# Performance work log

Hardware: AMD Instinct MI355X
Metric: run time of the kernel (lower is better)

## Reference

```python
import jax, jax.numpy as jnp
import numpy as np

EMBED_DIM = 300
HIDDEN = 128
N_CLS = 20
N_NODES = 100000
N_EDGES = 1600000
N_GRAPHS = 512
EPSILON = 1e-06


def setup_inputs() -> dict:
    key = jax.random.key(0)
    ks = jax.random.split(key, 10)
    x_fp16 = jax.random.normal(ks[0], (N_NODES, EMBED_DIM), dtype=jnp.float16)
    ei = jax.random.randint(ks[1], (2, N_EDGES), 0, N_NODES, dtype=jnp.int32)
    batch = jnp.sort(jax.random.randint(ks[2], (N_NODES,), 0, N_GRAPHS, dtype=jnp.int32))
    mask = jax.random.randint(ks[3], (N_NODES,), 0, 2, dtype=jnp.int32).astype(jnp.bool_)
    def glorot(k, fan_in, fan_out):
        s = (6.0 / (fan_in + fan_out)) ** 0.5
        return jax.random.uniform(k, (fan_in, fan_out), jnp.float32, -s, s)
    return {
        "x_fp16": x_fp16, "ei": ei, "batch": batch, "mask": mask,
        "W1": glorot(ks[4], EMBED_DIM, HIDDEN), "b1": jnp.zeros((HIDDEN,), jnp.float32),
        "W2": glorot(ks[5], HIDDEN, HIDDEN), "b2": jnp.zeros((HIDDEN,), jnp.float32),
        "Wout": glorot(ks[6], HIDDEN, N_CLS), "bout": jnp.zeros((N_CLS,), jnp.float32),
    }


def gcn_conv(x, W, b, src, dst, n):
    # PyG GCNConv: x' = D^{-1/2} (A + I) D^{-1/2} (x W) + b
    h = x @ W  # [N, out]
    loop = jnp.arange(n, dtype=src.dtype)
    s = jnp.concatenate([src, loop])
    d = jnp.concatenate([dst, loop])
    deg = jax.ops.segment_sum(jnp.ones_like(d, dtype=h.dtype), d, num_segments=n)
    dinv = jax.lax.rsqrt(deg)  # deg >= 1 thanks to self-loops
    norm = dinv[s] * dinv[d]  # [E+N]
    msg = h[s] * norm[:, None]
    return jax.ops.segment_sum(msg, d, num_segments=n) + b


def reference(x_fp16, ei, batch, mask, W1, b1, W2, b2, Wout, bout):
    n = x_fp16.shape[0]
    src, dst = ei[0], ei[1]
    x = x_fp16.astype(jnp.float32)
    x = jax.nn.relu(gcn_conv(x, W1, b1, src, dst, n))
    x = jax.nn.relu(gcn_conv(x, W2, b2, src, dst, n))
    m = mask.astype(jnp.float32)[:, None]  # [N,1]
    ent_sum = jax.ops.segment_sum(x * m, batch, num_segments=N_GRAPHS)  # [G,H]
    ent_cnt = jax.ops.segment_sum(m, batch, num_segments=N_GRAPHS)  # [G,1]
    doc_vec = ent_sum / (ent_cnt + EPSILON)
    # fallback: mean over all nodes when a graph has no masked entities
    node_sum = jax.ops.segment_sum(x, batch, num_segments=N_GRAPHS)
    node_cnt = jax.ops.segment_sum(jnp.ones((n, 1), jnp.float32), batch, num_segments=N_GRAPHS)
    mean_pool = node_sum / jnp.maximum(node_cnt, 1.0)
    zero = ent_cnt < EPSILON  # [G,1]
    doc_vec = jnp.where(zero, mean_pool, doc_vec)
    return jax.nn.log_softmax(doc_vec @ Wout + bout, axis=1)
```

## Files before the change

kernel.cpp:

```cpp
#include <hip/hip_runtime.h>
#include <hip/hip_fp16.h>

#define NN 100000
#define NE 1600000
#define DIM 300
#define HID 128
#define NC 20
#define NG 512
#define NBK 196
#define BCH 4096

typedef _Float16 h8 __attribute__((ext_vector_type(8)));
typedef float f4 __attribute__((ext_vector_type(4)));

union pack16 { float4 v; __half2 h2[4]; };

__device__ __forceinline__ __half tohalf(float v) {
  if (!(v == v)) v = 0.f;
  v = fminf(fmaxf(v, -60000.f), 60000.f);
  return __float2half(v);
}

__device__ __forceinline__ float load_x(const void* xraw, size_t o, int mode) {
  float v;
  if (mode == 2) v = ((const float*)xraw)[o];
  else {
    unsigned short u = ((const unsigned short*)xraw)[o];
    if (mode == 1) { union { unsigned w; float f; } c; c.w = ((unsigned)u) << 16; v = c.f; }
    else { union { unsigned short s; _Float16 h; } c; c.s = u; v = (float)c.h; }
  }
  if (!(v == v)) v = 0.f;
  return fminf(fmaxf(v, -1e4f), 1e4f);
}


__global__ void k_probe_modes(const unsigned short* __restrict__ xu, unsigned* __restrict__ diag) {
  int b = blockIdx.x, t = threadIdx.x;
  int mode = b % 3, chunk = b / 3;
  float m = 0.f;
  if (mode == 0) {
    int base = chunk * 16384;
    for (int j = t; j < 16384; j += 256) {
      union { unsigned short s; _Float16 h; } c; c.s = xu[base + j];
      float v = fabsf((float)c.h);
      if (v == v && v < 65000.f) m = fmaxf(m, v);
    }
  } else if (mode == 1) {
    int base = chunk * 16384;
    for (int j = t; j < 16384; j += 256) {
      union { unsigned w; float f; } c; c.w = ((unsigned)xu[base + j]) << 16;
      float v = fabsf(c.f);
      if (v == v && v < 1e30f) m = fmaxf(m, v);
    }
  } else {
    const float* xf = (const float*)xu;
    int base = chunk * 8192;
    for (int j = t; j < 8192; j += 256) {
      float v = fabsf(xf[base + j]);
      if (v == v && v < 1e30f) m = fmaxf(m, v);
    }
  }
  for (int off = 32; off; off >>= 1) m = fmaxf(m, __shfl_xor(m, off));
  if ((t & 63) == 0) atomicMax(&diag[20 + mode], __float_as_uint(m));
}

__global__ void k_probe_umax(const unsigned* __restrict__ p, unsigned* __restrict__ slot) {
  __shared__ unsigned red[256];
  int t = threadIdx.x; unsigned m = 0;
  for (int j = t; j < 25000; j += 256) m = max(m, p[j]);
  red[t] = m; __syncthreads();
  for (int off = 128; off; off >>= 1) { if (t < off) red[t] = max(red[t], red[t + off]); __syncthreads(); }
  if (t == 0) *slot = red[0];
}

__global__ void k_probe_ei(const int* __restrict__ e32, unsigned* __restrict__ slot) {
  int i = blockIdx.x * blockDim.x + threadIdx.x;
  int stride = gridDim.x * blockDim.x;
  unsigned z = 0;
  for (; i < 50000; i += stride) if (e32[2 * i + 1] == 0) z++;
  atomicAdd(slot, z);
}

__global__ void k_decide(const unsigned* __restrict__ diag, int* __restrict__ flags) {
  float M16 = __uint_as_float(diag[20]);
  float M32 = __uint_as_float(diag[21]);
  float Mf  = __uint_as_float(diag[22]);
  int xmode = 3;
  if      (Mf  > 3.f && Mf  < 8.f) xmode = 2;
  else if (M32 > 3.f && M32 < 8.f) xmode = 1;
  else if (M16 > 3.f && M16 < 8.f) xmode = 0;
  flags[0] = xmode;
  unsigned uA = diag[24], uB = diag[25];
  bool Ab = (uA >= 32u && uA < 1024u), Bb = (uB >= 32u && uB < 1024u);
  int swap = -1;
  if (Ab && !Bb) swap = 0;
  else if (Bb && !Ab) swap = 1;
  int mint = -1;
  if (swap >= 0) {
    unsigned um = (swap == 0) ? uB : uA;
    if (um <= 1u) mint = 1;
    else if (um >= 65536u) mint = 0;
  }
  flags[2] = (swap == 1) ? 1 : 0;
  flags[1] = (mint == 1) ? 1 : 0;
  flags[4] = (swap >= 0 && mint >= 0) ? 1 : 0;
  flags[3] = (diag[26] >= 49990u) ? 1 : 0;
}


__global__ void k_bhist(const int* __restrict__ e32, const int* __restrict__ flags,
                        int* __restrict__ bcnt) {
  __shared__ int hist[NBK];
  int e64 = flags[3];
  int t = threadIdx.x;
  for (int j = t; j < NBK; j += 256) hist[j] = 0;
  __syncthreads();
  int i = blockIdx.x * blockDim.x + t;
  int stride = gridDim.x * blockDim.x;
  for (; i < NE; i += stride) {
    int s = e64 ? e32[2 * i] : e32[i];
    int d = e64 ? e32[2 * NE + 2 * i] : e32[NE + i];
    if ((unsigned)s < (unsigned)NN && (unsigned)d < (unsigned)NN)
      atomicAdd(&hist[d >> 9], 1);
  }
  __syncthreads();
  for (int j = t; j < NBK; j += 256) if (hist[j]) atomicAdd(&bcnt[j], hist[j]);
}

__global__ void k_bscan(const int* __restrict__ bcnt, int* __restrict__ boff,
                        int* __restrict__ bcur) {
  if (blockIdx.x == 0 && threadIdx.x == 0) {
    int run = 0;
    for (int j = 0; j < NBK; j++) { boff[j] = run; bcur[j] = run; run += bcnt[j]; }
    boff[NBK] = run;
  }
}

__global__ __launch_bounds__(256)
void k_bscatter(const int* __restrict__ e32, const int* __restrict__ flags,
                int* __restrict__ bcur, unsigned* __restrict__ ebuf) {
  __shared__ uint2 stage[BCH];
  __shared__ int hist[NBK];
  __shared__ int lbase[NBK];
  __shared__ int lcur[NBK];
  int e64 = flags[3];
  int t = threadIdx.x;
  for (int j = t; j < NBK; j += 256) { hist[j] = 0; lcur[j] = 0; }
  __syncthreads();
  int start = blockIdx.x * BCH;
  int n = NE - start; if (n > BCH) n = BCH;
  for (int i = t; i < n; i += 256) {
    int idx = start + i;
    int s = e64 ? e32[2 * idx] : e32[idx];
    int d = e64 ? e32[2 * NE + 2 * idx] : e32[NE + idx];
    bool ok = ((unsigned)s < (unsigned)NN) && ((unsigned)d < (unsigned)NN);
    stage[i] = make_uint2(ok ? (unsigned)s : 0xFFFFFFFFu, (unsigned)(ok ? d : 0));
    if (ok) atomicAdd(&hist[d >> 9], 1);
  }
  __syncthreads();
  for (int j = t; j < NBK; j += 256) if (hist[j] > 0) lbase[j] = atomicAdd(&bcur[j], hist[j]);
  __syncthreads();
  for (int i = t; i < n; i += 256) {
    unsigned s = stage[i].x;
    if (s == 0xFFFFFFFFu) continue;
    int d = (int)stage[i].y;
    int b = d >> 9;
    int o = atomicAdd(&lcur[b], 1);
    ebuf[lbase[b] + o] = (s << 9) | (unsigned)(d & 511);
  }
}

__global__ __launch_bounds__(256)
void k_bfinal(const unsigned* __restrict__ ebuf, const int* __restrict__ boff,
              int* __restrict__ row_off, float* __restrict__ dinv, int* __restrict__ csr) {
  __shared__ int ldeg[512];
  __shared__ int lcur[512];
  int b = blockIdx.x, t = threadIdx.x;
  int base = b * 512;
  int nn = NN - base; if (nn > 512) nn = 512;
  for (int j = t; j < 512; j += 256) ldeg[j] = 0;
  __syncthreads();
  int s0 = boff[b], s1 = boff[b + 1];
  for (int e = s0 + t; e < s1; e += 256) atomicAdd(&ldeg[ebuf[e] & 511], 1);
  __syncthreads();
  if (t == 0) {
    int run = s0;
    for (int i = 0; i < nn; i++) { lcur[i] = run; row_off[base + i] = run; run += ldeg[i]; }
    if (b == gridDim.x - 1) row_off[NN] = run;
  }
  __syncthreads();
  for (int j = t; j < nn; j += 256) dinv[base + j] = rsqrtf((float)ldeg[j] + 1.0f);
  for (int e = s0 + t; e < s1; e += 256) {
    unsigned v = ebuf[e];
    int p = atomicAdd(&lcur[v & 511], 1);
    csr[p] = (int)(v >> 9);
  }
}


__global__ void k_gstart(const int* __restrict__ A, const int* __restrict__ B,
                         const int* __restrict__ flags, int* __restrict__ gstart) {
  const int* batch = flags[2] ? B : A;
  int g = blockIdx.x * blockDim.x + threadIdx.x;
  if (g > NG) return;
  if (g == NG) { gstart[NG] = NN; return; }
  int lo = 0, hi = NN;
  while (lo < hi) { int mid = (lo + hi) >> 1; if (batch[mid] < g) lo = mid + 1; else hi = mid; }
  gstart[g] = lo;
}


__global__ void k_prep(const float* __restrict__ W1, const float* __restrict__ W2,
                       _Float16* __restrict__ w1f, _Float16* __restrict__ w2f) {
  int idx = blockIdx.x * blockDim.x + threadIdx.x;
  const int S1 = 10 * 8 * 64 * 8;
  const int S2 = 4 * 8 * 64 * 8;
  if (idx < S1) {
    int j = idx & 7, l = (idx >> 3) & 63, nt = (idx >> 9) & 7, kc = idx >> 12;
    int k = kc * 32 + ((l >> 4) << 3) + j;
    int n = nt * 16 + (l & 15);
    w1f[idx] = (k < DIM) ? (_Float16)W1[k * HID + n] : (_Float16)0.f;
  } else if (idx < S1 + S2) {
    int q = idx - S1;
    int j = q & 7, l = (q >> 3) & 63, nt = (q >> 9) & 7, kc = q >> 12;
    int k = kc * 32 + ((l >> 4) << 3) + j;
    int n = nt * 16 + (l & 15);
    w2f[q] = (_Float16)W2[k * HID + n];
  }
}


#define XST 328

__global__ __launch_bounds__(256)
void k_gemm1_mfma(const void* __restrict__ Ain, const _Float16* __restrict__ bfrag,
                  const float* __restrict__ dinv, const int* __restrict__ flags,
                  __half* __restrict__ outg) {
  __shared__ _Float16 xs[64 * XST];
  const int mode = flags[0] & 3;
  int tid = threadIdx.x;
  int w = tid >> 6, l = tid & 63;
  int rowbase = blockIdx.x * 64;
  int k0base = (l >> 4) << 3;
  int cb = l & 15;

  for (int t = tid; t < 640; t += 256) {
    int rl = t / 10, j = t - rl * 10;
    *(unsigned*)&xs[rl * XST + 300 + j * 2] = 0u;
  }

  if (mode == 2) {
    const float* xf = (const float*)Ain;
    for (int c = tid; c < 64 * 75; c += 256) {
      int rl = c / 75, k = (c - rl * 75) * 4;
      int r = rowbase + rl;
      _Float16 o0 = 0, o1 = 0, o2 = 0, o3 = 0;
      if (r < NN) {
        float4 fv = *(const float4*)(xf + (size_t)r * DIM + k);
        o0 = (_Float16)fv.x; o1 = (_Float16)fv.y; o2 = (_Float16)fv.z; o3 = (_Float16)fv.w;
      }
      _Float16* p = &xs[rl * XST + k];
      p[0] = o0; p[1] = o1; p[2] = o2; p[3] = o3;
    }
  } else {
    const unsigned short* xu = (const unsigned short*)Ain;
    uint2 regs[19];
    #pragma unroll
    for (int it = 0; it < 19; it++) {
      int c = tid + it * 256;
      uint2 u = make_uint2(0u, 0u);
      if (c < 64 * 75) {
        int rl = c / 75, k = (c - rl * 75) * 4;
        int r = rowbase + rl;
        if (r < NN) u = *(const uint2*)(xu + (size_t)r * DIM + k);
      }
      regs[it] = u;
    }
    __builtin_amdgcn_sched_barrier(0);
    #pragma unroll
    for (int it = 0; it < 19; it++) {
      int c = tid + it * 256;
      if (c >= 64 * 75) continue;
      int rl = c / 75, k = (c - rl * 75) * 4;
      uint2 u = regs[it];
      unsigned short s0 = u.x & 0xFFFF, s1 = u.x >> 16, s2 = u.y & 0xFFFF, s3 = u.y >> 16;
      _Float16 o0, o1, o2, o3;
      if (mode == 1) {
        union { unsigned w_; float f; } c0, c1, c2, c3;
        c0.w_ = ((unsigned)s0) << 16; c1.w_ = ((unsigned)s1) << 16;
        c2.w_ = ((unsigned)s2) << 16; c3.w_ = ((unsigned)s3) << 16;
        o0 = (_Float16)c0.f; o1 = (_Float16)c1.f; o2 = (_Float16)c2.f; o3 = (_Float16)c3.f;
      } else {
        union { unsigned short s; _Float16 h; } d0, d1, d2, d3;
        d0.s = s0; d1.s = s1; d2.s = s2; d3.s = s3;
        o0 = d0.h; o1 = d1.h; o2 = d2.h; o3 = d3.h;
      }
      _Float16* p = &xs[rl * XST + k];
      p[0] = o0; p[1] = o1; p[2] = o2; p[3] = o3;
    }
  }
  __syncthreads();

  f4 acc[4][2];
  f4 zero = {0.f, 0.f, 0.f, 0.f};
  #pragma unroll
  for (int rg = 0; rg < 4; rg++) { acc[rg][0] = zero; acc[rg][1] = zero; }

  #pragma unroll
  for (int kc = 0; kc < 10; kc++) {
    int ko = kc * 32 + k0base;
    h8 a0 = *(const h8*)&xs[(0 * 16 + cb) * XST + ko];
    h8 a1 = *(const h8*)&xs[(1 * 16 + cb) * XST + ko];
    h8 a2 = *(const h8*)&xs[(2 * 16 + cb) * XST + ko];
    h8 a3 = *(const h8*)&xs[(3 * 16 + cb) * XST + ko];
    #pragma unroll
    for (int ntl = 0; ntl < 2; ntl++) {
      int nt = w * 2 + ntl;
      h8 bv = *(const h8*)&bfrag[(((kc << 3) + nt) * 64 + l) * 8];
      acc[0][ntl] = __builtin_amdgcn_mfma_f32_16x16x32_f16(a0, bv, acc[0][ntl], 0, 0, 0);
      acc[1][ntl] = __builtin_amdgcn_mfma_f32_16x16x32_f16(a1, bv, acc[1][ntl], 0, 0, 0);
      acc[2][ntl] = __builtin_amdgcn_mfma_f32_16x16x32_f16(a2, bv, acc[2][ntl], 0, 0, 0);
      acc[3][ntl] = __builtin_amdgcn_mfma_f32_16x16x32_f16(a3, bv, acc[3][ntl], 0, 0, 0);
    }
  }

  int rquad = (l >> 4) << 2;
  #pragma unroll
  for (int rg = 0; rg < 4; rg++) {
    #pragma unroll
    for (int i = 0; i < 4; i++) {
      int r = rowbase + rg * 16 + rquad + i;
      if (r >= NN) continue;
      float dv = dinv[r];
      __half* orow = outg + (size_t)r * HID;
      orow[(w * 2 + 0) * 16 + cb] = tohalf(acc[rg][0][i] * dv);
      orow[(w * 2 + 1) * 16 + cb] = tohalf(acc[rg][1][i] * dv);
    }
  }
}


__global__ __launch_bounds__(256)
void k_gemm2_mfma(const __half* __restrict__ Ain, const _Float16* __restrict__ bfrag,
                  const float* __restrict__ dinv, __half* __restrict__ outg) {
  __shared__ _Float16 xs[64 * 136];
  int tid = threadIdx.x;
  int w = tid >> 6, l = tid & 63;
  int rowbase = blockIdx.x * 64;
  int k0base = (l >> 4) << 3;
  int cb = l & 15;

  {
    h8 regs[4];
    #pragma unroll
    for (int it = 0; it < 4; it++) {
      int c = tid + it * 256;
      int rl = c >> 4, k = (c & 15) * 8;
      int r = rowbase + rl;
      h8 v = {};
      if (r < NN) v = *(const h8*)((const _Float16*)Ain + (size_t)r * HID + k);
      regs[it] = v;
    }
    __builtin_amdgcn_sched_barrier(0);
    #pragma unroll
    for (int it = 0; it < 4; it++) {
      int c = tid + it * 256;
      int rl = c >> 4, k = (c & 15) * 8;
      *(h8*)&xs[rl * 136 + k] = regs[it];
    }
  }
  __syncthreads();

  f4 acc[4][2];
  f4 zero = {0.f, 0.f, 0.f, 0.f};
  #pragma unroll
  for (int rg = 0; rg < 4; rg++) { acc[rg][0] = zero; acc[rg][1] = zero; }

  #pragma unroll
  for (int kc = 0; kc < 4; kc++) {
    int ko = kc * 32 + k0base;
    h8 a0 = *(const h8*)&xs[(0 * 16 + cb) * 136 + ko];
    h8 a1 = *(const h8*)&xs[(1 * 16 + cb) * 136 + ko];
    h8 a2 = *(const h8*)&xs[(2 * 16 + cb) * 136 + ko];
    h8 a3 = *(const h8*)&xs[(3 * 16 + cb) * 136 + ko];
    #pragma unroll
    for (int ntl = 0; ntl < 2; ntl++) {
      int nt = w * 2 + ntl;
      h8 bv = *(const h8*)&bfrag[(((kc << 3) + nt) * 64 + l) * 8];
      acc[0][ntl] = __builtin_amdgcn_mfma_f32_16x16x32_f16(a0, bv, acc[0][ntl], 0, 0, 0);
      acc[1][ntl] = __builtin_amdgcn_mfma_f32_16x16x32_f16(a1, bv, acc[1][ntl], 0, 0, 0);
      acc[2][ntl] = __builtin_amdgcn_mfma_f32_16x16x32_f16(a2, bv, acc[2][ntl], 0, 0, 0);
      acc[3][ntl] = __builtin_amdgcn_mfma_f32_16x16x32_f16(a3, bv, acc[3][ntl], 0, 0, 0);
    }
  }

  int rquad = (l >> 4) << 2;
  #pragma unroll
  for (int rg = 0; rg < 4; rg++) {
    #pragma unroll
    for (int i = 0; i < 4; i++) {
      int r = rowbase + rg * 16 + rquad + i;
      if (r >= NN) continue;
      float dv = dinv[r];
      __half* orow = outg + (size_t)r * HID;
      orow[(w * 2 + 0) * 16 + cb] = tohalf(acc[rg][0][i] * dv);
      orow[(w * 2 + 1) * 16 + cb] = tohalf(acc[rg][1][i] * dv);
    }
  }
}


__global__ __launch_bounds__(256)
void k_agg(const __half* __restrict__ g, const float* __restrict__ dinv,
           const int* __restrict__ row_off, const int* __restrict__ csr,
           const float* __restrict__ bias, __half* __restrict__ out) {
  int tid = threadIdx.x;
  int node = blockIdx.x * 4 + (tid >> 6);
  int l = tid & 63;
  if (node >= NN) return;
  int grp = l >> 4;
  int cl  = l & 15;
  size_t coff = (size_t)cl * 8;

  float a0 = 0.f, a1 = 0.f, a2 = 0.f, a3 = 0.f, a4 = 0.f, a5 = 0.f, a6 = 0.f, a7 = 0.f;
  pack16 r;

  #define ACCUM() do { \
    float2 f0 = __half22float2(r.h2[0]); \
    float2 f1 = __half22float2(r.h2[1]); \
    float2 f2 = __half22float2(r.h2[2]); \
    float2 f3 = __half22float2(r.h2[3]); \
    a0 += f0.x; a1 += f0.y; a2 += f1.x; a3 += f1.y; \
    a4 += f2.x; a5 += f2.y; a6 += f3.x; a7 += f3.y; } while (0)

  int e0 = row_off[node], e1 = row_off[node + 1];
  int e = e0 + grp;
  for (; e + 4 < e1; e += 8) {
    int s1 = csr[e], s2 = csr[e + 4];
    pack16 rA, rB;
    rA.v = *(const float4*)(g + (size_t)s1 * HID + coff);
    rB.v = *(const float4*)(g + (size_t)s2 * HID + coff);
    r = rA; ACCUM();
    r = rB; ACCUM();
  }
  if (e < e1) {
    int s1 = csr[e];
    r.v = *(const float4*)(g + (size_t)s1 * HID + coff);
    ACCUM();
  }
  if (grp == 0) {
    r.v = *(const float4*)(g + (size_t)node * HID + coff);
    ACCUM();
  }
  #undef ACCUM

  a0 += __shfl_xor(a0, 16); a1 += __shfl_xor(a1, 16); a2 += __shfl_xor(a2, 16); a3 += __shfl_xor(a3, 16);
  a4 += __shfl_xor(a4, 16); a5 += __shfl_xor(a5, 16); a6 += __shfl_xor(a6, 16); a7 += __shfl_xor(a7, 16);
  a0 += __shfl_xor(a0, 32); a1 += __shfl_xor(a1, 32); a2 += __shfl_xor(a2, 32); a3 += __shfl_xor(a3, 32);
  a4 += __shfl_xor(a4, 32); a5 += __shfl_xor(a5, 32); a6 += __shfl_xor(a6, 32); a7 += __shfl_xor(a7, 32);

  if (grp == 0) {
    float di = dinv[node];
    const float* bp = bias + coff;
    pack16 w;
    w.h2[0] = __floats2half2_rn(fmaxf(a0 * di + bp[0], 0.f), fmaxf(a1 * di + bp[1], 0.f));
    w.h2[1] = __floats2half2_rn(fmaxf(a2 * di + bp[2], 0.f), fmaxf(a3 * di + bp[3], 0.f));
    w.h2[2] = __floats2half2_rn(fmaxf(a4 * di + bp[4], 0.f), fmaxf(a5 * di + bp[5], 0.f));
    w.h2[3] = __floats2half2_rn(fmaxf(a6 * di + bp[6], 0.f), fmaxf(a7 * di + bp[7], 0.f));
    *(float4*)(out + (size_t)node * HID + coff) = w.v;
  }
}


__global__ __launch_bounds__(256)
void k_pool(const __half* __restrict__ o2, const void* __restrict__ Araw, const void* __restrict__ Braw,
            const int* __restrict__ gstart, const int* __restrict__ flags,
            float* __restrict__ doc) {
  __shared__ float lex[4][HID];
  __shared__ float lnx[4][HID];
  __shared__ int lec[4];
  int gid = blockIdx.x, tid = threadIdx.x;
  int wv = tid >> 6, l = tid & 63;
  int grp = l >> 4, cl = l & 15;
  size_t coff = (size_t)cl * 8;
  const int mint = flags[1];
  const void* mraw = flags[2] ? Araw : Braw;
  const unsigned char* m8 = (const unsigned char*)mraw;
  const int* m32 = (const int*)mraw;
  int s = gstart[gid], e = gstart[gid + 1];

  float ex[8], nx[8];
  #pragma unroll
  for (int j = 0; j < 8; j++) { ex[j] = 0.f; nx[j] = 0.f; }
  int ec = 0;

  for (int n = s + wv * 4 + grp; n < e; n += 16) {
    pack16 r;
    r.v = *(const float4*)(o2 + (size_t)n * HID + coff);
    float2 f0 = __half22float2(r.h2[0]);
    float2 f1 = __half22float2(r.h2[1]);
    float2 f2 = __half22float2(r.h2[2]);
    float2 f3 = __half22float2(r.h2[3]);
    float t0 = f0.x, t1 = f0.y, t2 = f1.x, t3 = f1.y;
    float t4 = f2.x, t5 = f2.y, t6 = f3.x, t7 = f3.y;
    nx[0] += t0; nx[1] += t1; nx[2] += t2; nx[3] += t3;
    nx[4] += t4; nx[5] += t5; nx[6] += t6; nx[7] += t7;
    bool mv = mint ? (m32[n] != 0) : (m8[n] != 0);
    if (mv) {
      ex[0] += t0; ex[1] += t1; ex[2] += t2; ex[3] += t3;
      ex[4] += t4; ex[5] += t5; ex[6] += t6; ex[7] += t7;
      ec++;
    }
  }
  #pragma unroll
  for (int j = 0; j < 8; j++) {
    ex[j] += __shfl_xor(ex[j], 16); ex[j] += __shfl_xor(ex[j], 32);
    nx[j] += __shfl_xor(nx[j], 16); nx[j] += __shfl_xor(nx[j], 32);
  }
  ec += __shfl_xor(ec, 16); ec += __shfl_xor(ec, 32);

  if (grp == 0) {
    #pragma unroll
    for (int j = 0; j < 8; j++) { lex[wv][cl * 8 + j] = ex[j]; lnx[wv][cl * 8 + j] = nx[j]; }
    if (cl == 0) lec[wv] = ec;
  }
  __syncthreads();
  if (tid < HID) {
    float exT = lex[0][tid] + lex[1][tid] + lex[2][tid] + lex[3][tid];
    float nxT = lnx[0][tid] + lnx[1][tid] + lnx[2][tid] + lnx[3][tid];
    int ecT = lec[0] + lec[1] + lec[2] + lec[3];
    int cnt = e - s;
    float dv;
    if (ecT > 0) dv = exT / ((float)ecT + 1e-6f);
    else dv = (cnt > 0) ? nxT / (float)cnt : 0.f;
    doc[gid * HID + tid] = dv;
  }
}

__global__ __launch_bounds__(64)
void k_out(const float* __restrict__ doc, const float* __restrict__ Wout,
           const float* __restrict__ bout, float* __restrict__ out) {
  __shared__ float dv[HID];
  int gid = blockIdx.x, l = threadIdx.x;
  dv[l] = doc[gid * HID + l];
  dv[l + 64] = doc[gid * HID + l + 64];
  __syncthreads();
  float logit = -1e30f;
  if (l < NC) {
    float acc = bout[l];
    for (int k = 0; k < HID; k++) acc += dv[k] * Wout[k * NC + l];
    logit = acc;
  }
  float m = logit;
  for (int off = 32; off; off >>= 1) m = fmaxf(m, __shfl_xor(m, off));
  float ex = (l < NC) ? expf(logit - m) : 0.f;
  float ssum = ex;
  for (int off = 32; off; off >>= 1) ssum += __shfl_xor(ssum, off);
  if (l < NC) out[gid * NC + l] = (logit - m) - logf(ssum);
}

__global__ void k_fail(float* __restrict__ out, float enc) {
  int i = blockIdx.x * blockDim.x + threadIdx.x;
  if (i < NG * NC) out[i] = -enc;
}


extern "C" void kernel_launch(void* const* d_in, const int* in_sizes, int n_in,
                              void* d_out, int out_size, void* d_ws, size_t ws_size,
                              hipStream_t stream) {
  int ix = -1, iei = -1, iA = -1, iB = -1, iW1 = -1, ib1 = -1, iW2 = -1, ib2 = -1, iWo = -1, ibo = -1;
  for (int i = 0; i < n_in; i++) {
    int s = in_sizes[i];
    if (s == 30000000) ix = i;
    else if (s == 3200000) iei = i;
    else if (s == 100000) { if (iA < 0) iA = i; else iB = i; }
    else if (s == 38400) iW1 = i;
    else if (s == 16384) iW2 = i;
    else if (s == 2560) iWo = i;
    else if (s == 20) ibo = i;
    else if (s == 128) { if (ib1 < 0) ib1 = i; else ib2 = i; }
  }
  float* out = (float*)d_out;
  int miss = -1;
  if (ix < 0) miss = 0; else if (iei < 0) miss = 1; else if (iA < 0 || iB < 0) miss = 2;
  else if (iW1 < 0) miss = 3; else if (ib1 < 0 || ib2 < 0) miss = 4; else if (iW2 < 0) miss = 5;
  else if (iWo < 0) miss = 6; else if (ibo < 0) miss = 7;
  if (miss >= 0) {
    k_fail<<<(NG * NC + 255) / 256, 256, 0, stream>>>(out, 8192.f + 64.f * (float)miss);
    return;
  }
  const void* x = d_in[ix];
  const int* e32 = (const int*)d_in[iei];
  const void* Araw = d_in[iA];
  const void* Braw = d_in[iB];
  const float* W1 = (const float*)d_in[iW1];
  const float* b1 = (const float*)d_in[ib1];
  const float* W2 = (const float*)d_in[iW2];
  const float* b2 = (const float*)d_in[ib2];
  const float* Wout = (const float*)d_in[iWo];
  const float* bout = (const float*)d_in[ibo];

  char* ws = (char*)d_ws;
  size_t off = 0;
  auto alloc = [&](size_t bytes) -> char* {
    char* p = ws + off; off += (bytes + 255) & ~(size_t)255; return p;
  };
  float* dinv   = (float*)alloc((size_t)NN * 4);
  int* row_off  = (int*)alloc((size_t)(NN + 1) * 4);
  int* csr      = (int*)alloc((size_t)NE * 4);
  int* bcnt     = (int*)alloc((size_t)NBK * 4);
  int* boff     = (int*)alloc((size_t)(NBK + 1) * 4);
  int* bcur     = (int*)alloc((size_t)NBK * 4);
  int* gstart   = (int*)alloc((size_t)(NG + 1) * 4);
  int* flags    = (int*)alloc(8 * 4);
  _Float16* w1f = (_Float16*)alloc(40960 * 2);
  _Float16* w2f = (_Float16*)alloc(16384 * 2);
  __half* gbuf  = (__half*)alloc((size_t)NN * HID * 2);
  __half* obuf  = (__half*)alloc((size_t)NN * HID * 2);
  float* doc    = (float*)alloc((size_t)NG * HID * 4);
  unsigned* diag = (unsigned*)alloc(64 * 4);
  unsigned* ebuf = (unsigned*)gbuf;

  hipMemsetAsync(bcnt, 0, (size_t)NBK * 4, stream);
  hipMemsetAsync(diag, 0, 64 * 4, stream);

  k_probe_modes<<<96, 256, 0, stream>>>((const unsigned short*)x, diag);
  k_probe_umax<<<1, 256, 0, stream>>>((const unsigned*)Araw, &diag[24]);
  k_probe_umax<<<1, 256, 0, stream>>>((const unsigned*)Braw, &diag[25]);
  k_probe_ei<<<64, 256, 0, stream>>>(e32, &diag[26]);
  k_decide<<<1, 1, 0, stream>>>(diag, flags);

  k_prep<<<(57344 + 255) / 256, 256, 0, stream>>>(W1, W2, w1f, w2f);
  k_bhist<<<1024, 256, 0, stream>>>(e32, flags, bcnt);
  k_bscan<<<1, 64, 0, stream>>>(bcnt, boff, bcur);
  k_bscatter<<<(NE + BCH - 1) / BCH, 256, 0, stream>>>(e32, flags, bcur, ebuf);
  k_bfinal<<<NBK, 256, 0, stream>>>(ebuf, boff, row_off, dinv, csr);
  k_gstart<<<(NG + 1 + 63) / 64, 64, 0, stream>>>((const int*)Araw, (const int*)Braw, flags, gstart);

  k_gemm1_mfma<<<(NN + 63) / 64, 256, 0, stream>>>(x, w1f, dinv, flags, gbuf);
  k_agg<<<NN / 4, 256, 0, stream>>>(gbuf, dinv, row_off, csr, b1, obuf);
  k_gemm2_mfma<<<(NN + 63) / 64, 256, 0, stream>>>(obuf, w2f, dinv, gbuf);
  k_agg<<<NN / 4, 256, 0, stream>>>(gbuf, dinv, row_off, csr, b2, obuf);

  k_pool<<<NG, 256, 0, stream>>>(obuf, Araw, Braw, gstart, flags, doc);
  k_out<<<NG, 64, 0, stream>>>(doc, Wout, bout, out);
}
```

Before: 355.2 us.

## Split gemm1 K dimension into two LDS halves to halve shared memory

The first-layer MFMA GEMM now stages the 300-wide input row tile in two halves (160 then 140 plus zero padding) through a half-size LDS buffer, with an extra barrier between phases. This cuts LDS per block roughly in half, and drops the 19-register prefetch array, so more blocks can be resident per CU to hide global load latency. In exchange, the second half's loads are serialized behind the first half's MFMAs, and the preload-all-then-convert scheme that batched global loads is gone.

```diff
diff --git a/kernel.cpp b/kernel.cpp
--- a/kernel.cpp
+++ b/kernel.cpp
@@ -31,6 +31,26 @@
   }
   if (!(v == v)) v = 0.f;
   return fminf(fmaxf(v, -1e4f), 1e4f);
+}
+
+__device__ __forceinline__ void cvt4(const void* Ain, size_t off, int mode, _Float16* o) {
+  if (mode == 2) {
+    float4 fv = *(const float4*)((const float*)Ain + off);
+    o[0] = (_Float16)fv.x; o[1] = (_Float16)fv.y; o[2] = (_Float16)fv.z; o[3] = (_Float16)fv.w;
+  } else {
+    uint2 u = *(const uint2*)((const unsigned short*)Ain + off);
+    unsigned short s0 = u.x & 0xFFFF, s1 = u.x >> 16, s2 = u.y & 0xFFFF, s3 = u.y >> 16;
+    if (mode == 1) {
+      union { unsigned w; float f; } c0, c1, c2, c3;
+      c0.w = ((unsigned)s0) << 16; c1.w = ((unsigned)s1) << 16;
+      c2.w = ((unsigned)s2) << 16; c3.w = ((unsigned)s3) << 16;
+      o[0] = (_Float16)c0.f; o[1] = (_Float16)c1.f; o[2] = (_Float16)c2.f; o[3] = (_Float16)c3.f;
+    } else {
+      union { unsigned short s; _Float16 h; } d0, d1, d2, d3;
+      d0.s = s0; d1.s = s1; d2.s = s2; d3.s = s3;
+      o[0] = d0.h; o[1] = d1.h; o[2] = d2.h; o[3] = d3.h;
+    }
+  }
 }
 
 
@@ -230,13 +250,13 @@
 }
 
 
-#define XST 328
+#define XS1 168
 
 __global__ __launch_bounds__(256)
 void k_gemm1_mfma(const void* __restrict__ Ain, const _Float16* __restrict__ bfrag,
                   const float* __restrict__ dinv, const int* __restrict__ flags,
                   __half* __restrict__ outg) {
-  __shared__ _Float16 xs[64 * XST];
+  __shared__ _Float16 xs[64 * XS1];
   const int mode = flags[0] & 3;
   int tid = threadIdx.x;
   int w = tid >> 6, l = tid & 63;
@@ -244,75 +264,65 @@
   int k0base = (l >> 4) << 3;
   int cb = l & 15;
 
-  for (int t = tid; t < 640; t += 256) {
-    int rl = t / 10, j = t - rl * 10;
-    *(unsigned*)&xs[rl * XST + 300 + j * 2] = 0u;
-  }
-
-  if (mode == 2) {
-    const float* xf = (const float*)Ain;
-    for (int c = tid; c < 64 * 75; c += 256) {
-      int rl = c / 75, k = (c - rl * 75) * 4;
-      int r = rowbase + rl;
-      _Float16 o0 = 0, o1 = 0, o2 = 0, o3 = 0;
-      if (r < NN) {
-        float4 fv = *(const float4*)(xf + (size_t)r * DIM + k);
-        o0 = (_Float16)fv.x; o1 = (_Float16)fv.y; o2 = (_Float16)fv.z; o3 = (_Float16)fv.w;
-      }
-      _Float16* p = &xs[rl * XST + k];
-      p[0] = o0; p[1] = o1; p[2] = o2; p[3] = o3;
-    }
-  } else {
-    const unsigned short* xu = (const unsigned short*)Ain;
-    uint2 regs[19];
-    #pragma unroll
-    for (int it = 0; it < 19; it++) {
-      int c = tid + it * 256;
-      uint2 u = make_uint2(0u, 0u);
-      if (c < 64 * 75) {
-        int rl = c / 75, k = (c - rl * 75) * 4;
-        int r = rowbase + rl;
-        if (r < NN) u = *(const uint2*)(xu + (size_t)r * DIM + k);
-      }
-      regs[it] = u;
-    }
-    __builtin_amdgcn_sched_barrier(0);
-    #pragma unroll
-    for (int it = 0; it < 19; it++) {
-      int c = tid + it * 256;
-      if (c >= 64 * 75) continue;
-      int rl = c / 75, k = (c - rl * 75) * 4;
-      uint2 u = regs[it];
-      unsigned short s0 = u.x & 0xFFFF, s1 = u.x >> 16, s2 = u.y & 0xFFFF, s3 = u.y >> 16;
-      _Float16 o0, o1, o2, o3;
-      if (mode == 1) {
-        union { unsigned w_; float f; } c0, c1, c2, c3;
-        c0.w_ = ((unsigned)s0) << 16; c1.w_ = ((unsigned)s1) << 16;
-        c2.w_ = ((unsigned)s2) << 16; c3.w_ = ((unsigned)s3) << 16;
-        o0 = (_Float16)c0.f; o1 = (_Float16)c1.f; o2 = (_Float16)c2.f; o3 = (_Float16)c3.f;
-      } else {
-        union { unsigned short s; _Float16 h; } d0, d1, d2, d3;
-        d0.s = s0; d1.s = s1; d2.s = s2; d3.s = s3;
-        o0 = d0.h; o1 = d1.h; o2 = d2.h; o3 = d3.h;
-      }
-      _Float16* p = &xs[rl * XST + k];
-      p[0] = o0; p[1] = o1; p[2] = o2; p[3] = o3;
-    }
-  }
-  __syncthreads();
-
   f4 acc[4][2];
   f4 zero = {0.f, 0.f, 0.f, 0.f};
   #pragma unroll
   for (int rg = 0; rg < 4; rg++) { acc[rg][0] = zero; acc[rg][1] = zero; }
 
   #pragma unroll
-  for (int kc = 0; kc < 10; kc++) {
+  for (int it = 0; it < 10; it++) {
+    int c = tid + it * 256;
+    int rl = c / 40, kk = (c - rl * 40) * 4;
+    int r = rowbase + rl;
+    _Float16 o[4] = {0, 0, 0, 0};
+    if (r < NN) cvt4(Ain, (size_t)r * DIM + kk, mode, o);
+    _Float16* p = &xs[rl * XS1 + kk];
+    p[0] = o[0]; p[1] = o[1]; p[2] = o[2]; p[3] = o[3];
+  }
+  __syncthreads();
+  #pragma unroll
+  for (int kc = 0; kc < 5; kc++) {
     int ko = kc * 32 + k0base;
-    h8 a0 = *(const h8*)&xs[(0 * 16 + cb) * XST + ko];
-    h8 a1 = *(const h8*)&xs[(1 * 16 + cb) * XST + ko];
-    h8 a2 = *(const h8*)&xs[(2 * 16 + cb) * XST + ko];
-    h8 a3 = *(const h8*)&xs[(3 * 16 + cb) * XST + ko];
+    h8 a0 = *(const h8*)&xs[(0 * 16 + cb) * XS1 + ko];
+    h8 a1 = *(const h8*)&xs[(1 * 16 + cb) * XS1 + ko];
+    h8 a2 = *(const h8*)&xs[(2 * 16 + cb) * XS1 + ko];
+    h8 a3 = *(const h8*)&xs[(3 * 16 + cb) * XS1 + ko];
+    #pragma unroll
+    for (int ntl = 0; ntl < 2; ntl++) {
+      int nt = w * 2 + ntl;
+      h8 bv = *(const h8*)&bfrag[(((kc << 3) + nt) * 64 + l) * 8];
+      acc[0][ntl] = __builtin_amdgcn_mfma_f32_16x16x32_f16(a0, bv, acc[0][ntl], 0, 0, 0);
+      acc[1][ntl] = __builtin_amdgcn_mfma_f32_16x16x32_f16(a1, bv, acc[1][ntl], 0, 0, 0);
+      acc[2][ntl] = __builtin_amdgcn_mfma_f32_16x16x32_f16(a2, bv, acc[2][ntl], 0, 0, 0);
+      acc[3][ntl] = __builtin_amdgcn_mfma_f32_16x16x32_f16(a3, bv, acc[3][ntl], 0, 0, 0);
+    }
+  }
+  __syncthreads();
+
+  for (int t2 = tid; t2 < 64 * 10; t2 += 256) {
+    int rl = t2 / 10, j = t2 - rl * 10;
+    *(unsigned*)&xs[rl * XS1 + 140 + j * 2] = 0u;
+  }
+  #pragma unroll
+  for (int it = 0; it < 9; it++) {
+    int c = tid + it * 256;
+    if (c < 64 * 35) {
+      int rl = c / 35, kk = (c - rl * 35) * 4;
+      int r = rowbase + rl;
+      _Float16 o[4] = {0, 0, 0, 0};
+      if (r < NN) cvt4(Ain, (size_t)r * DIM + 160 + kk, mode, o);
+      _Float16* p = &xs[rl * XS1 + kk];
+      p[0] = o[0]; p[1] = o[1]; p[2] = o[2]; p[3] = o[3];
+    }
+  }
+  __syncthreads();
+  #pragma unroll
+  for (int kc = 5; kc < 10; kc++) {
+    int ko = (kc - 5) * 32 + k0base;
+    h8 a0 = *(const h8*)&xs[(0 * 16 + cb) * XS1 + ko];
+    h8 a1 = *(const h8*)&xs[(1 * 16 + cb) * XS1 + ko];
+    h8 a2 = *(const h8*)&xs[(2 * 16 + cb) * XS1 + ko];
+    h8 a3 = *(const h8*)&xs[(3 * 16 + cb) * XS1 + ko];
     #pragma unroll
     for (int ntl = 0; ntl < 2; ntl++) {
       int nt = w * 2 + ntl;
```

After: 349.8 us. About the same (-1.5%).
